# Performance work log

Measured on AMD Instinct MI355X. Metric: run time of the kernel, lower is better.

## Reference

```python
import jax, jax.numpy as jnp
import numpy as np

N = 8192
STEPS = 10        # num_propagation_steps
ALPHA = 0.5       # self-retention parameter
LR = 0.01         # learning_rate for the M update
EPS = 1e-10


def setup_inputs() -> dict:
    key = jax.random.key(0)
    k1, k2 = jax.random.split(key)
    adj_matrix = jax.random.uniform(k1, (N, N), dtype=jnp.float32)  # dense non-negative adjacency
    positive_nodes = jax.random.bernoulli(k2, 0.5, (N,)).astype(jnp.float32)  # binary labels
    M = jnp.ones((N, N), dtype=jnp.float32)  # nn.Parameter initialized to ones
    return {"adj_matrix": adj_matrix, "positive_nodes": positive_nodes, "M": M}


def _propagation_loss(adj, pos):
    # degree_matrix @ adj @ degree_matrix with diagonal degree matrix ==
    # row/column scaling by deg^{-1/2} (same math, no O(N^3) diag GEMMs)
    d = jnp.power(adj.sum(axis=1), -0.5)          # [N]
    diffusion = d[:, None] * adj * d[None, :]     # [N, N]
    cp = jnp.stack([1.0 - pos, pos], axis=1)      # [N, 2] class posterior

    def step(cp, _):
        cp = ALPHA * (diffusion @ cp) + (1.0 - ALPHA) * cp
        return cp, None

    cp, _ = jax.lax.scan(step, cp, None, length=STEPS)
    # mean of -log(1 - neg_prob + eps) over nodes where positive_nodes == 1
    neg = cp[:, 0]
    loss = -(pos * jnp.log(1.0 - neg + EPS)).sum() / pos.sum()
    return loss


def reference(adj_matrix, positive_nodes, M):
    loss = _propagation_loss(adj_matrix, positive_nodes)
    # In the original, loss.backward() populates M.grad; since the loss does not
    # depend on M, dLoss/dM == 0, so M_new = M - LR * 0 = M (math-equivalent).
    updated_adj = M * adj_matrix
    return updated_adj, loss
```

## Files before the change

kernel.cpp:

```cpp
#include <hip/hip_runtime.h>
#include <hip/hip_bf16.h>

#define NN 8192
constexpr int   STEPS = 10;
constexpr float ALPHA = 0.5f;
constexpr float EPSV  = 1e-10f;

typedef float f32x2 __attribute__((ext_vector_type(2)));
typedef float f32x4 __attribute__((ext_vector_type(4)));

static __device__ __forceinline__ unsigned int f2bf(float f) {
    unsigned int u = __float_as_uint(f);
    return (u + 0x7FFFu + ((u >> 16) & 1u)) >> 16;
}
static __device__ __forceinline__ float bf2f(unsigned int h) {
    return __uint_as_float(h << 16);
}

__global__ __launch_bounds__(256) void k_fused_prep(
        const float* __restrict__ adj, const float* __restrict__ M,
        float* __restrict__ out, unsigned char* __restrict__ a8,
        float* __restrict__ rowsum) {
    const int row = blockIdx.x;
    const int t   = threadIdx.x;
    const float* arow = adj + (size_t)row * NN;
    const float* mrow = M   + (size_t)row * NN;
    float*       orow = out + (size_t)row * NN;
    unsigned char* brow = a8 + (size_t)row * NN;
    float acc = 0.0f;
#pragma unroll
    for (int g = 0; g < 2; ++g) {
        f32x4 v[4], m[4];
#pragma unroll
        for (int k = 0; k < 4; ++k) {
            const int j = (g * 4 + k) * 1024 + t * 4;
            v[k] = __builtin_nontemporal_load((const f32x4*)(arow + j));
        }
#pragma unroll
        for (int k = 0; k < 4; ++k) {
            const int j = (g * 4 + k) * 1024 + t * 4;
            m[k] = __builtin_nontemporal_load((const f32x4*)(mrow + j));
        }
#pragma unroll
        for (int k = 0; k < 4; ++k) {
            const int j = (g * 4 + k) * 1024 + t * 4;
            f32x4 r = v[k] * m[k];
            __builtin_nontemporal_store(r, (f32x4*)(orow + j));
            acc += (v[k].x + v[k].y) + (v[k].z + v[k].w);
            int p = __builtin_amdgcn_cvt_pk_fp8_f32(v[k].x, v[k].y, 0, false);
            p     = __builtin_amdgcn_cvt_pk_fp8_f32(v[k].z, v[k].w, p, true);
            *(unsigned int*)(brow + j) = (unsigned int)p;
        }
    }
#pragma unroll
    for (int o = 32; o > 0; o >>= 1) acc += __shfl_down(acc, o);
    __shared__ float red[4];
    if ((t & 63) == 0) red[t >> 6] = acc;
    __syncthreads();
    if (t == 0) rowsum[row] = (red[0] + red[1]) + (red[2] + red[3]);
}

__global__ __launch_bounds__(256) void k_rowsum(
        const float* __restrict__ adj, float* __restrict__ rowsum) {
    const int row = blockIdx.x;
    const int t   = threadIdx.x;
    const float* arow = adj + (size_t)row * NN;
    float acc = 0.0f;
#pragma unroll
    for (int c = 0; c < 8; ++c) {
        const int j = c * 1024 + t * 4;
        float4 v = *(const float4*)(arow + j);
        acc += (v.x + v.y) + (v.z + v.w);
    }
#pragma unroll
    for (int o = 32; o > 0; o >>= 1) acc += __shfl_down(acc, o);
    __shared__ float red[4];
    if ((t & 63) == 0) red[t >> 6] = acc;
    __syncthreads();
    if (t == 0) rowsum[row] = (red[0] + red[1]) + (red[2] + red[3]);
}

__global__ __launch_bounds__(256) void k_init(
        const float* __restrict__ rowsum, const float* __restrict__ pos,
        float* __restrict__ d, float* __restrict__ x,
        unsigned short* __restrict__ zbf, float* __restrict__ zf) {
    const int i = blockIdx.x * 256 + threadIdx.x;
    const float dv = rsqrtf(rowsum[i]);
    const float xv = 1.0f - pos[i];
    const float zv = dv * xv;
    d[i] = dv;
    x[i] = xv;
    zbf[i] = (unsigned short)f2bf(zv);
    zf[i] = zv;
}

__global__ __launch_bounds__(256) void k_step_fp8(
        const unsigned char* __restrict__ a8, const float* __restrict__ d,
        const float* __restrict__ xin, const unsigned short* __restrict__ zin,
        float* __restrict__ xout, unsigned short* __restrict__ zout) {
    const int r0 = blockIdx.x * 4;
    const int t  = threadIdx.x;
    const int j  = t * 32;

    uint4 pa[4][2];
#pragma unroll
    for (int r = 0; r < 4; ++r) {
        const unsigned char* arow = a8 + (size_t)(r0 + r) * NN + j;
        pa[r][0] = *(const uint4*)(arow);
        pa[r][1] = *(const uint4*)(arow + 16);
    }
    uint4 zp[4];
#pragma unroll
    for (int k = 0; k < 4; ++k)
        zp[k] = *(const uint4*)(zin + j + 8 * k);

    float acc0 = 0.0f, acc1 = 0.0f, acc2 = 0.0f, acc3 = 0.0f;
#pragma unroll
    for (int h = 0; h < 2; ++h) {
        float zf[16];
#pragma unroll
        for (int k = 0; k < 2; ++k) {
            uint4 q = zp[2 * h + k];
            zf[k * 8 + 0] = bf2f(q.x & 0xFFFFu); zf[k * 8 + 1] = bf2f(q.x >> 16);
            zf[k * 8 + 2] = bf2f(q.y & 0xFFFFu); zf[k * 8 + 3] = bf2f(q.y >> 16);
            zf[k * 8 + 4] = bf2f(q.z & 0xFFFFu); zf[k * 8 + 5] = bf2f(q.z >> 16);
            zf[k * 8 + 6] = bf2f(q.w & 0xFFFFu); zf[k * 8 + 7] = bf2f(q.w >> 16);
        }
#pragma unroll
        for (int r = 0; r < 4; ++r) {
            const uint4 p = pa[r][h];
            unsigned int w[4] = {p.x, p.y, p.z, p.w};
            float a = 0.0f;
#pragma unroll
            for (int wi = 0; wi < 4; ++wi) {
                f32x2 lo = __builtin_amdgcn_cvt_pk_f32_fp8((int)w[wi], false);
                f32x2 hi = __builtin_amdgcn_cvt_pk_f32_fp8((int)w[wi], true);
                a = fmaf(lo[0], zf[wi * 4 + 0], a);
                a = fmaf(lo[1], zf[wi * 4 + 1], a);
                a = fmaf(hi[0], zf[wi * 4 + 2], a);
                a = fmaf(hi[1], zf[wi * 4 + 3], a);
            }
            if (r == 0) acc0 += a; else if (r == 1) acc1 += a;
            else if (r == 2) acc2 += a; else acc3 += a;
        }
    }
#pragma unroll
    for (int o = 32; o > 0; o >>= 1) {
        acc0 += __shfl_down(acc0, o);
        acc1 += __shfl_down(acc1, o);
        acc2 += __shfl_down(acc2, o);
        acc3 += __shfl_down(acc3, o);
    }
    __shared__ float red[4][4];
    if ((t & 63) == 0) {
        const int w = t >> 6;
        red[0][w] = acc0; red[1][w] = acc1; red[2][w] = acc2; red[3][w] = acc3;
    }
    __syncthreads();
    if (t < 4) {
        const int row = r0 + t;
        const float y  = (red[t][0] + red[t][1]) + (red[t][2] + red[t][3]);
        const float dv = d[row];
        const float xn = ALPHA * dv * y + (1.0f - ALPHA) * xin[row];
        xout[row] = xn;
        zout[row] = (unsigned short)f2bf(dv * xn);
    }
}

__global__ __launch_bounds__(256) void k_step_f32(
        const float* __restrict__ adj, const float* __restrict__ d,
        const float* __restrict__ xin, const float* __restrict__ zin,
        float* __restrict__ xout, float* __restrict__ zout) {
    const int row = blockIdx.x;
    const int t   = threadIdx.x;
    const float* arow = adj + (size_t)row * NN;
    float acc = 0.0f;
#pragma unroll
    for (int c = 0; c < 8; ++c) {
        const int j = c * 1024 + t * 4;
        float4 a = *(const float4*)(arow + j);
        float4 z = *(const float4*)(zin + j);
        acc = fmaf(a.x, z.x, acc); acc = fmaf(a.y, z.y, acc);
        acc = fmaf(a.z, z.z, acc); acc = fmaf(a.w, z.w, acc);
    }
#pragma unroll
    for (int o = 32; o > 0; o >>= 1) acc += __shfl_down(acc, o);
    __shared__ float red[4];
    if ((t & 63) == 0) red[t >> 6] = acc;
    __syncthreads();
    if (t == 0) {
        const float y  = (red[0] + red[1]) + (red[2] + red[3]);
        const float dv = d[row];
        const float xn = ALPHA * dv * y + (1.0f - ALPHA) * xin[row];
        xout[row] = xn;
        zout[row] = dv * xn;
    }
}

__global__ __launch_bounds__(256) void k_mul(
        const float* __restrict__ adj, const float* __restrict__ M,
        float* __restrict__ out) {
    size_t i = ((size_t)blockIdx.x * blockDim.x + threadIdx.x) * 4;
    const size_t stride = (size_t)gridDim.x * blockDim.x * 4;
    const size_t total = (size_t)NN * NN;
    for (; i < total; i += stride) {
        float4 a = *(const float4*)(adj + i);
        float4 m = *(const float4*)(M + i);
        float4 r;
        r.x = a.x * m.x; r.y = a.y * m.y; r.z = a.z * m.z; r.w = a.w * m.w;
        *(float4*)(out + i) = r;
    }
}

__global__ __launch_bounds__(1024) void k_loss(
        const float* __restrict__ pos, const float* __restrict__ xfin,
        float* __restrict__ out) {
    const int t = threadIdx.x;
    float sn = 0.0f, sd = 0.0f;
#pragma unroll
    for (int c = 0; c < 8; ++c) {
        const int i4 = c * 1024 + t;
        float4 p = *(const float4*)(pos  + i4 * 4);
        float4 x = *(const float4*)(xfin + i4 * 4);
        sn += p.x * logf(1.0f - x.x + EPSV);
        sn += p.y * logf(1.0f - x.y + EPSV);
        sn += p.z * logf(1.0f - x.z + EPSV);
        sn += p.w * logf(1.0f - x.w + EPSV);
        sd += (p.x + p.y) + (p.z + p.w);
    }
#pragma unroll
    for (int o = 32; o > 0; o >>= 1) {
        sn += __shfl_down(sn, o);
        sd += __shfl_down(sd, o);
    }
    __shared__ float rn[16], rd[16];
    if ((t & 63) == 0) { rn[t >> 6] = sn; rd[t >> 6] = sd; }
    __syncthreads();
    if (t == 0) {
        float n = 0.0f, dd = 0.0f;
#pragma unroll
        for (int k = 0; k < 16; ++k) { n += rn[k]; dd += rd[k]; }
        out[0] = -n / dd;
    }
}

extern "C" void kernel_launch(void* const* d_in, const int* in_sizes, int n_in,
                              void* d_out, int out_size, void* d_ws, size_t ws_size,
                              hipStream_t stream) {
    const float* adj = (const float*)d_in[0];
    const float* pos = (const float*)d_in[1];
    const float* M   = (const float*)d_in[2];
    float* out = (float*)d_out;

    char* ws = (char*)d_ws;
    float* d_vec  = (float*)(ws + 0);
    float* rowsum = (float*)(ws + 32768);
    float* x_a    = (float*)(ws + 65536);
    float* x_b    = (float*)(ws + 98304);
    unsigned short* zb_a = (unsigned short*)(ws + 131072);
    unsigned short* zb_b = (unsigned short*)(ws + 163840);
    float* zf_a   = (float*)(ws + 196608);
    float* zf_b   = (float*)(ws + 229376);
    unsigned char* a8 = (unsigned char*)(ws + 262144);

    const size_t need_fp8 = 262144 + (size_t)NN * NN;
    const bool use_fp8 = (ws_size >= need_fp8);

    if (use_fp8) {
        k_fused_prep<<<NN, 256, 0, stream>>>(adj, M, out, a8, rowsum);
    } else {
        k_rowsum<<<NN, 256, 0, stream>>>(adj, rowsum);
    }

    k_init<<<NN / 256, 256, 0, stream>>>(rowsum, pos, d_vec, x_a, zb_a, zf_a);

    float* xi = x_a; float* xo = x_b;
    unsigned short* zbi = zb_a; unsigned short* zbo = zb_b;
    float* zfi = zf_a; float* zfo = zf_b;
    for (int s = 0; s < STEPS; ++s) {
        if (use_fp8) {
            k_step_fp8<<<NN / 4, 256, 0, stream>>>(a8, d_vec, xi, zbi, xo, zbo);
            unsigned short* tz = zbi; zbi = zbo; zbo = tz;
        } else {
            k_step_f32<<<NN, 256, 0, stream>>>(adj, d_vec, xi, zfi, xo, zfo);
            float* tz = zfi; zfi = zfo; zfo = tz;
        }
        float* t = xi; xi = xo; xo = t;
    }

    if (!use_fp8) {
        k_mul<<<2048, 256, 0, stream>>>(adj, M, out);
    }
    k_loss<<<1, 1024, 0, stream>>>(pos, xi, out + (size_t)NN * NN);
}
```

Before: 261.0 us.

## Fuse init, propagation steps and loss into one cooperative persistent kernel

Replaces the init kernel, the ten per-step fp8 matvec launches and the loss kernel with a single cooperative-launch kernel of 1024 blocks. Each block handles 8 rows and uses grid.sync between steps. This removes per-launch overhead and tail effects across roughly 12 launches. In exchange it adds grid-wide barrier cost, requires all 1024 blocks to be co-resident (checked by an occupancy query), and falls back to the old path otherwise.

```diff
diff --git a/kernel.cpp b/kernel.cpp
--- a/kernel.cpp
+++ b/kernel.cpp
@@ -1,5 +1,8 @@
 #include <hip/hip_runtime.h>
 #include <hip/hip_bf16.h>
+#include <hip/hip_cooperative_groups.h>
+
+namespace cg = cooperative_groups;
 
 #define NN 8192
 constexpr int   STEPS = 10;
@@ -94,6 +97,124 @@
     zf[i] = zv;
 }
 
+__global__ __launch_bounds__(256, 4) void k_coop(
+        const unsigned char* __restrict__ a8, const float* __restrict__ rowsum,
+        const float* __restrict__ pos, float* __restrict__ d,
+        float* __restrict__ x_a, float* __restrict__ x_b,
+        unsigned short* __restrict__ zb_a, unsigned short* __restrict__ zb_b,
+        float* __restrict__ loss_out) {
+    cg::grid_group grid = cg::this_grid();
+    const int t = threadIdx.x;
+    const int b = blockIdx.x;
+    __shared__ float red[8][4];
+
+    if (b < NN / 256) {
+        const int i = b * 256 + t;
+        const float dv = rsqrtf(rowsum[i]);
+        const float xv = 1.0f - pos[i];
+        d[i]   = dv;
+        x_a[i] = xv;
+        zb_a[i] = (unsigned short)f2bf(dv * xv);
+    }
+    grid.sync();
+
+    float* xi = x_a; float* xo = x_b;
+    unsigned short* zi = zb_a; unsigned short* zo = zb_b;
+    const int j  = t * 32;
+    const int r0 = b * 8;
+
+    for (int s = 0; s < STEPS; ++s) {
+        float zf[32];
+#pragma unroll
+        for (int k = 0; k < 4; ++k) {
+            const uint4 q = *(const uint4*)(zi + j + 8 * k);
+            zf[k * 8 + 0] = bf2f(q.x & 0xFFFFu); zf[k * 8 + 1] = bf2f(q.x >> 16);
+            zf[k * 8 + 2] = bf2f(q.y & 0xFFFFu); zf[k * 8 + 3] = bf2f(q.y >> 16);
+            zf[k * 8 + 4] = bf2f(q.z & 0xFFFFu); zf[k * 8 + 5] = bf2f(q.z >> 16);
+            zf[k * 8 + 6] = bf2f(q.w & 0xFFFFu); zf[k * 8 + 7] = bf2f(q.w >> 16);
+        }
+#pragma unroll
+        for (int h2 = 0; h2 < 2; ++h2) {
+            uint4 pa[4][2];
+#pragma unroll
+            for (int r = 0; r < 4; ++r) {
+                const unsigned char* arow = a8 + (size_t)(r0 + h2 * 4 + r) * NN + j;
+                pa[r][0] = *(const uint4*)(arow);
+                pa[r][1] = *(const uint4*)(arow + 16);
+            }
+            float acc0 = 0.0f, acc1 = 0.0f, acc2 = 0.0f, acc3 = 0.0f;
+#pragma unroll
+            for (int r = 0; r < 4; ++r) {
+                const unsigned int w[8] = {pa[r][0].x, pa[r][0].y, pa[r][0].z, pa[r][0].w,
+                                           pa[r][1].x, pa[r][1].y, pa[r][1].z, pa[r][1].w};
+                float a = 0.0f;
+#pragma unroll
+                for (int wi = 0; wi < 8; ++wi) {
+                    f32x2 lo = __builtin_amdgcn_cvt_pk_f32_fp8((int)w[wi], false);
+                    f32x2 hi = __builtin_amdgcn_cvt_pk_f32_fp8((int)w[wi], true);
+                    a = fmaf(lo[0], zf[wi * 4 + 0], a);
+                    a = fmaf(lo[1], zf[wi * 4 + 1], a);
+                    a = fmaf(hi[0], zf[wi * 4 + 2], a);
+                    a = fmaf(hi[1], zf[wi * 4 + 3], a);
+                }
+                if (r == 0) acc0 += a; else if (r == 1) acc1 += a;
+                else if (r == 2) acc2 += a; else acc3 += a;
+            }
+#pragma unroll
+            for (int o = 32; o > 0; o >>= 1) {
+                acc0 += __shfl_down(acc0, o);
+                acc1 += __shfl_down(acc1, o);
+                acc2 += __shfl_down(acc2, o);
+                acc3 += __shfl_down(acc3, o);
+            }
+            if ((t & 63) == 0) {
+                const int w = t >> 6;
+                red[h2 * 4 + 0][w] = acc0; red[h2 * 4 + 1][w] = acc1;
+                red[h2 * 4 + 2][w] = acc2; red[h2 * 4 + 3][w] = acc3;
+            }
+        }
+        __syncthreads();
+        if (t < 8) {
+            const int row = r0 + t;
+            const float y  = (red[t][0] + red[t][1]) + (red[t][2] + red[t][3]);
+            const float dv = d[row];
+            const float xn = ALPHA * dv * y + (1.0f - ALPHA) * xi[row];
+            xo[row] = xn;
+            zo[row] = (unsigned short)f2bf(dv * xn);
+        }
+        grid.sync();
+        { float* tx = xi; xi = xo; xo = tx; }
+        { unsigned short* tz = zi; zi = zo; zo = tz; }
+    }
+
+    if (b == 0) {
+        float sn = 0.0f, sd = 0.0f;
+#pragma unroll
+        for (int c = 0; c < 8; ++c) {
+            const int i4 = c * 256 + t;
+            const float4 p  = *(const float4*)(pos + i4 * 4);
+            const float4 xv = *(const float4*)(xi  + i4 * 4);
+            sn += p.x * logf(1.0f - xv.x + EPSV);
+            sn += p.y * logf(1.0f - xv.y + EPSV);
+            sn += p.z * logf(1.0f - xv.z + EPSV);
+            sn += p.w * logf(1.0f - xv.w + EPSV);
+            sd += (p.x + p.y) + (p.z + p.w);
+        }
+#pragma unroll
+        for (int o = 32; o > 0; o >>= 1) {
+            sn += __shfl_down(sn, o);
+            sd += __shfl_down(sd, o);
+        }
+        if ((t & 63) == 0) { red[0][t >> 6] = sn; red[1][t >> 6] = sd; }
+        __syncthreads();
+        if (t == 0) {
+            const float n  = (red[0][0] + red[0][1]) + (red[0][2] + red[0][3]);
+            const float dd = (red[1][0] + red[1][1]) + (red[1][2] + red[1][3]);
+            loss_out[0] = -n / dd;
+        }
+    }
+}
+
 __global__ __launch_bounds__(256) void k_step_fp8(
         const unsigned char* __restrict__ a8, const float* __restrict__ d,
         const float* __restrict__ xin, const unsigned short* __restrict__ zin,
@@ -266,30 +387,50 @@
     const size_t need_fp8 = 262144 + (size_t)NN * NN;
     const bool use_fp8 = (ws_size >= need_fp8);
 
+    static int s_coop = -1;
+    if (s_coop < 0) {
+        int nb = 0, ncu = 0;
+        hipError_t e1 = hipOccupancyMaxActiveBlocksPerMultiprocessor(&nb, k_coop, 256, 0);
+        hipError_t e2 = hipDeviceGetAttribute(&ncu, hipDeviceAttributeMultiprocessorCount, 0);
+        s_coop = (e1 == hipSuccess && e2 == hipSuccess && nb * ncu >= 1024) ? 1 : 0;
+    }
+
     if (use_fp8) {
         k_fused_prep<<<NN, 256, 0, stream>>>(adj, M, out, a8, rowsum);
     } else {
         k_rowsum<<<NN, 256, 0, stream>>>(adj, rowsum);
     }
 
-    k_init<<<NN / 256, 256, 0, stream>>>(rowsum, pos, d_vec, x_a, zb_a, zf_a);
-
-    float* xi = x_a; float* xo = x_b;
-    unsigned short* zbi = zb_a; unsigned short* zbo = zb_b;
-    float* zfi = zf_a; float* zfo = zf_b;
-    for (int s = 0; s < STEPS; ++s) {
-        if (use_fp8) {
-            k_step_fp8<<<NN / 4, 256, 0, stream>>>(a8, d_vec, xi, zbi, xo, zbo);
-            unsigned short* tz = zbi; zbi = zbo; zbo = tz;
-        } else {
-            k_step_f32<<<NN, 256, 0, stream>>>(adj, d_vec, xi, zfi, xo, zfo);
-            float* tz = zfi; zfi = zfo; zfo = tz;
-        }
-        float* t = xi; xi = xo; xo = t;
-    }
-
-    if (!use_fp8) {
-        k_mul<<<2048, 256, 0, stream>>>(adj, M, out);
-    }
-    k_loss<<<1, 1024, 0, stream>>>(pos, xi, out + (size_t)NN * NN);
-}
+    bool coop_done = false;
+    if (use_fp8 && s_coop == 1) {
+        float* lossp = out + (size_t)NN * NN;
+        void* args[9] = { (void*)&a8, (void*)&rowsum, (void*)&pos, (void*)&d_vec,
+                          (void*)&x_a, (void*)&x_b, (void*)&zb_a, (void*)&zb_b,
+                          (void*)&lossp };
+        if (hipLaunchCooperativeKernel((const void*)k_coop, dim3(1024), dim3(256),
+                                       args, 0, stream) == hipSuccess) {
+            coop_done = true;
+        }
+    }
+
+    if (!coop_done) {
+        k_init<<<NN / 256, 256, 0, stream>>>(rowsum, pos, d_vec, x_a, zb_a, zf_a);
+        float* xi = x_a; float* xo = x_b;
+        unsigned short* zbi = zb_a; unsigned short* zbo = zb_b;
+        float* zfi = zf_a; float* zfo = zf_b;
+        for (int s = 0; s < STEPS; ++s) {
+            if (use_fp8) {
+                k_step_fp8<<<NN / 4, 256, 0, stream>>>(a8, d_vec, xi, zbi, xo, zbo);
+                unsigned short* tz = zbi; zbi = zbo; zbo = tz;
+            } else {
+                k_step_f32<<<NN, 256, 0, stream>>>(adj, d_vec, xi, zfi, xo, zfo);
+                float* tz = zfi; zfi = zfo; zfo = tz;
+            }
+            float* t = xi; xi = xo; xo = t;
+        }
+        if (!use_fp8) {
+            k_mul<<<2048, 256, 0, stream>>>(adj, M, out);
+        }
+        k_loss<<<1, 1024, 0, stream>>>(pos, xi, out + (size_t)NN * NN);
+    }
+}
```

New measurement: 262.6 us. No clear change (+0.6%).

## Fuse propagation steps into persistent kernel with grid barrier and register-resident FP8 matrix

Applied to the files above, without the earlier changes.

Replaces the init kernel, ten per-step kernel launches and the loss kernel with one persistent kernel of 256 blocks. Each block keeps its 32 rows of the FP8 matrix in registers across all steps and exchanges the scaled bf16 vector through global memory with an atomic flag grid barrier. This removes repeated launch overhead and re-reading the 64MB FP8 matrix every step. The cost is heavy register pressure, possible spills, and reliance on all blocks being co-resident, which an occupancy check guards.

```diff
diff --git a/kernel.cpp b/kernel.cpp
--- a/kernel.cpp
+++ b/kernel.cpp
@@ -58,6 +58,143 @@
     if ((t & 63) == 0) red[t >> 6] = acc;
     __syncthreads();
     if (t == 0) rowsum[row] = (red[0] + red[1]) + (red[2] + red[3]);
+}
+
+#define CBLK  256
+#define CROWS 32
+
+static __device__ __forceinline__ void gbar(unsigned int* flags, unsigned int phase) {
+    __syncthreads();
+    if (threadIdx.x == 0)
+        __hip_atomic_store(&flags[blockIdx.x], phase, __ATOMIC_RELEASE,
+                           __HIP_MEMORY_SCOPE_AGENT);
+    while (__hip_atomic_load(&flags[threadIdx.x], __ATOMIC_ACQUIRE,
+                             __HIP_MEMORY_SCOPE_AGENT) < phase)
+        __builtin_amdgcn_s_sleep(1);
+    __syncthreads();
+}
+
+#define FMA_WORD(w, base)                                             \
+    { f32x2 lo = __builtin_amdgcn_cvt_pk_f32_fp8((int)(w), false);    \
+      f32x2 hi = __builtin_amdgcn_cvt_pk_f32_fp8((int)(w), true);     \
+      a0 = fmaf(lo[0], zf[(base) + 0], a0);                           \
+      a1 = fmaf(lo[1], zf[(base) + 1], a1);                           \
+      a0 = fmaf(hi[0], zf[(base) + 2], a0);                           \
+      a1 = fmaf(hi[1], zf[(base) + 3], a1); }
+
+__global__ __launch_bounds__(256, 1) void k_chain(
+        const unsigned char* __restrict__ a8, const float* __restrict__ rowsum,
+        const float* __restrict__ pos,
+        unsigned int* __restrict__ z_a, unsigned int* __restrict__ z_b,
+        unsigned int* __restrict__ flags, float* __restrict__ accs,
+        float* __restrict__ loss_out) {
+    const int t  = threadIdx.x;
+    const int b  = blockIdx.x;
+    const int r0 = b * CROWS;
+    __shared__ float xloc[CROWS], dloc[CROWS], ploc[CROWS];
+    __shared__ unsigned short zs[CROWS];
+    __shared__ float red[CROWS][4];
+
+    if (t < CROWS) {
+        const int row = r0 + t;
+        const float dv = rsqrtf(rowsum[row]);
+        const float pv = pos[row];
+        const float xv = 1.0f - pv;
+        dloc[t] = dv; ploc[t] = pv; xloc[t] = xv;
+        zs[t] = (unsigned short)f2bf(dv * xv);
+    }
+    __syncthreads();
+    if (t < CROWS / 2) {
+        unsigned int w = (unsigned)zs[2 * t] | ((unsigned)zs[2 * t + 1] << 16);
+        __hip_atomic_store(&z_a[r0 / 2 + t], w, __ATOMIC_RELAXED,
+                           __HIP_MEMORY_SCOPE_AGENT);
+    }
+    gbar(flags, 1u);
+
+    const int j = t * 32;
+    uint4 pa[CROWS][2];
+#pragma unroll
+    for (int r = 0; r < CROWS; ++r) {
+        const unsigned char* arow = a8 + (size_t)(r0 + r) * NN + j;
+        pa[r][0] = *(const uint4*)(arow);
+        pa[r][1] = *(const uint4*)(arow + 16);
+    }
+
+    const unsigned int* zi = z_a;
+    unsigned int*       zo = z_b;
+#pragma unroll 1
+    for (int s = 0; s < STEPS; ++s) {
+        float zf[32];
+#pragma unroll
+        for (int k = 0; k < 16; ++k) {
+            unsigned int q = __hip_atomic_load(&zi[(j >> 1) + k], __ATOMIC_RELAXED,
+                                               __HIP_MEMORY_SCOPE_AGENT);
+            zf[2 * k]     = bf2f(q & 0xFFFFu);
+            zf[2 * k + 1] = bf2f(q >> 16);
+        }
+        float acc[CROWS];
+#pragma unroll
+        for (int r = 0; r < CROWS; ++r) {
+            float a0 = 0.0f, a1 = 0.0f;
+            FMA_WORD(pa[r][0].x,  0) FMA_WORD(pa[r][0].y,  4)
+            FMA_WORD(pa[r][0].z,  8) FMA_WORD(pa[r][0].w, 12)
+            FMA_WORD(pa[r][1].x, 16) FMA_WORD(pa[r][1].y, 20)
+            FMA_WORD(pa[r][1].z, 24) FMA_WORD(pa[r][1].w, 28)
+            acc[r] = a0 + a1;
+        }
+#pragma unroll
+        for (int r = 0; r < CROWS; ++r) {
+#pragma unroll
+            for (int o = 32; o > 0; o >>= 1) acc[r] += __shfl_down(acc[r], o);
+        }
+        if ((t & 63) == 0) {
+            const int w = t >> 6;
+#pragma unroll
+            for (int r = 0; r < CROWS; ++r) red[r][w] = acc[r];
+        }
+        __syncthreads();
+        if (t < CROWS) {
+            const float y  = (red[t][0] + red[t][1]) + (red[t][2] + red[t][3]);
+            const float dv = dloc[t];
+            const float xn = ALPHA * dv * y + (1.0f - ALPHA) * xloc[t];
+            xloc[t] = xn;
+            zs[t] = (unsigned short)f2bf(dv * xn);
+        }
+        __syncthreads();
+        if (s < STEPS - 1) {
+            if (t < CROWS / 2) {
+                unsigned int w = (unsigned)zs[2 * t] | ((unsigned)zs[2 * t + 1] << 16);
+                __hip_atomic_store(&zo[r0 / 2 + t], w, __ATOMIC_RELAXED,
+                                   __HIP_MEMORY_SCOPE_AGENT);
+            }
+            gbar(flags, (unsigned)(2 + s));
+            const unsigned int* tz = zi; zi = zo; zo = (unsigned int*)tz;
+        }
+    }
+
+    if (t < CROWS) {
+        const float xn = xloc[t];
+        red[t][0] = ploc[t] * logf(1.0f - xn + EPSV);
+        red[t][1] = ploc[t];
+    }
+    __syncthreads();
+    if (t == 0) {
+        float n = 0.0f, dd = 0.0f;
+#pragma unroll
+        for (int r = 0; r < CROWS; ++r) { n += red[r][0]; dd += red[r][1]; }
+        atomicAdd(&accs[0], n);
+        atomicAdd(&accs[1], dd);
+        unsigned int tk = __hip_atomic_fetch_add((unsigned int*)&accs[2], 1u,
+                                                 __ATOMIC_ACQ_REL,
+                                                 __HIP_MEMORY_SCOPE_AGENT);
+        if (tk == CBLK - 1) {
+            float sn = __hip_atomic_load(&accs[0], __ATOMIC_RELAXED,
+                                         __HIP_MEMORY_SCOPE_AGENT);
+            float sd = __hip_atomic_load(&accs[1], __ATOMIC_RELAXED,
+                                         __HIP_MEMORY_SCOPE_AGENT);
+            loss_out[0] = -sn / sd;
+        }
+    }
 }
 
 __global__ __launch_bounds__(256) void k_rowsum(
@@ -259,12 +396,22 @@
     float* x_b    = (float*)(ws + 98304);
     unsigned short* zb_a = (unsigned short*)(ws + 131072);
     unsigned short* zb_b = (unsigned short*)(ws + 163840);
+    unsigned int* flags  = (unsigned int*)(ws + 196608);
+    float*        accs   = (float*)(ws + 196608 + 4096);
     float* zf_a   = (float*)(ws + 196608);
     float* zf_b   = (float*)(ws + 229376);
     unsigned char* a8 = (unsigned char*)(ws + 262144);
 
     const size_t need_fp8 = 262144 + (size_t)NN * NN;
     const bool use_fp8 = (ws_size >= need_fp8);
+
+    static int s_chain = -1;
+    if (s_chain < 0) {
+        int nb = 0, ncu = 0;
+        hipError_t e1 = hipOccupancyMaxActiveBlocksPerMultiprocessor(&nb, k_chain, 256, 0);
+        hipError_t e2 = hipDeviceGetAttribute(&ncu, hipDeviceAttributeMultiprocessorCount, 0);
+        s_chain = (e1 == hipSuccess && e2 == hipSuccess && nb >= 1 && nb * ncu >= CBLK) ? 1 : 0;
+    }
 
     if (use_fp8) {
         k_fused_prep<<<NN, 256, 0, stream>>>(adj, M, out, a8, rowsum);
@@ -272,8 +419,15 @@
         k_rowsum<<<NN, 256, 0, stream>>>(adj, rowsum);
     }
 
+    if (use_fp8 && s_chain == 1) {
+        hipMemsetAsync(flags, 0, 4096 + 64, stream);
+        k_chain<<<CBLK, 256, 0, stream>>>(a8, rowsum, pos,
+                                          (unsigned int*)zb_a, (unsigned int*)zb_b,
+                                          flags, accs, out + (size_t)NN * NN);
+        return;
+    }
+
     k_init<<<NN / 256, 256, 0, stream>>>(rowsum, pos, d_vec, x_a, zb_a, zf_a);
-
     float* xi = x_a; float* xo = x_b;
     unsigned short* zbi = zb_a; unsigned short* zbo = zb_b;
     float* zfi = zf_a; float* zfo = zf_b;
@@ -287,7 +441,6 @@
         }
         float* t = xi; xi = xo; xo = t;
     }
-
     if (!use_fp8) {
         k_mul<<<2048, 256, 0, stream>>>(adj, M, out);
     }
```

After: 261.5 us. Within noise of the previous version (+0.2%).
